# Kernel optimization log

Hardware: AMD Instinct MI355X
Metric: run time of the kernel (lower is better)

The kernel has to match this reference:

```python
import jax, jax.numpy as jnp
import numpy as np

N_DST = 100_000
N_SRC = 200_000
DEG = 16            # fixed avg degree -> E = N_DST*DEG
E = N_DST * DEG
P, K, W = 16, 256, 8  # num_parts, codebook entries, part width; feat_dim = P*W = 128
F_IN = P * W
F_OUT = 128


def setup_inputs() -> dict:
    key = jax.random.key(0)
    k1, k2, k3, k4, k5, k6, k7 = jax.random.split(key, 7)
    codes = jax.random.randint(k1, (N_SRC, P), 0, K, dtype=jnp.int32)
    indices = jax.random.randint(k2, (E,), 0, N_SRC, dtype=jnp.int32)
    indptr = (jnp.arange(N_DST + 1, dtype=jnp.int32) * DEG)
    h_self = jax.random.normal(k3, (N_DST, F_IN), dtype=jnp.float32)
    codebook = jax.random.normal(k4, (P, K, W), dtype=jnp.float32)
    W_neigh = jax.random.normal(k5, (F_OUT, F_IN), dtype=jnp.float32) * (1.0 / np.sqrt(F_IN))
    W_self = jax.random.normal(k6, (F_OUT, F_IN), dtype=jnp.float32) * (1.0 / np.sqrt(F_IN))
    b_self = jax.random.normal(k7, (F_OUT,), dtype=jnp.float32) * 0.01
    return {"codes": codes, "indices": indices, "indptr": indptr, "h_self": h_self,
            "codebook": codebook, "W_neigh": W_neigh, "W_self": W_self, "b_self": b_self}


def reference(codes, indices, indptr, h_self, codebook, W_neigh, W_self, b_self):
    n_dst = indptr.shape[0] - 1
    n_edges = indices.shape[0]
    # --- VQ decompress: codebook[p, codes[n, p]] -> [N_src, P, W] -> [N_src, F_IN]
    feat = codebook[jnp.arange(P)[None, :], codes]          # [N_src, P, W]
    feat = feat.reshape(feat.shape[0], F_IN)                # [N_src, F_IN]
    # --- CSR(CSC) mean SpMM over neighbors
    # dst id of each edge from indptr (jit-safe, static E)
    dst_ids = jnp.searchsorted(indptr, jnp.arange(n_edges, dtype=indptr.dtype), side="right") - 1
    gathered = feat[indices]                                 # [E, F_IN] (irregular gather)
    summed = jax.ops.segment_sum(gathered, dst_ids, num_segments=n_dst)  # [N_dst, F_IN]
    deg = jnp.diff(indptr).astype(summed.dtype)
    h_neigh = summed / jnp.maximum(deg, 1.0)[:, None]        # mean aggregation
    # --- linear combine: fc_neigh(h_neigh) + fc_self(h_self)
    rst = h_neigh @ W_neigh.T + h_self @ W_self.T + b_self[None, :]
    return rst
```

## Files before the change

kernel.cpp:

```cpp
#include <hip/hip_runtime.h>
#include <stdint.h>

constexpr int N_DST = 100000;
constexpr int N_SRC = 200000;
constexpr int DEG   = 16;
constexpr int PP    = 16;
constexpr int KK    = 256;
constexpr int WW    = 8;
constexpr int F_IN  = 128;
constexpr int F_OUT = 128;

typedef __attribute__((ext_vector_type(8))) short short8;
typedef __attribute__((ext_vector_type(4))) float floatx4;

__device__ __forceinline__ unsigned short f2bf(float f) {
    unsigned int u = __float_as_uint(f);
    unsigned int r = (u + 0x7FFFu + ((u >> 16) & 1u)) >> 16;
    return (unsigned short)r;
}
__device__ __forceinline__ float bf2f(unsigned int bits16) {
    return __uint_as_float(bits16 << 16);
}

constexpr int DT = 64;
constexpr int NT = (N_DST + DT - 1) / DT;
constexpr int LDS_STRIDE = 264;

__global__ __launch_bounds__(1024, 1) void fused_kernel(
    const int* __restrict__ codes, const int* __restrict__ indices,
    const float* __restrict__ codebook, const float* __restrict__ h_self,
    const float* __restrict__ Wn, const float* __restrict__ Ws,
    const float* __restrict__ b_self, float* __restrict__ out)
{
    __shared__ __align__(16) unsigned short scb[PP * KK * WW];
    __shared__ __align__(16) unsigned short hcat[DT][LDS_STRIDE];

    const int tid  = threadIdx.x;
    const int wv   = tid >> 6;
    const int lane = tid & 63;
    const int quad = lane >> 4;
    const int r    = lane & 15;
    const int p    = lane & 15;
    const int sub  = lane >> 4;

    {
        const float4* cb4 = (const float4*)codebook;
        ushort4* s4 = (ushort4*)scb;
        #pragma unroll
        for (int it = 0; it < 8; ++it) {
            const int i = tid + it * 1024;
            const float4 v = cb4[i];
            ushort4 w;
            w.x = f2bf(v.x); w.y = f2bf(v.y); w.z = f2bf(v.z); w.w = f2bf(v.w);
            s4[i] = w;
        }
    }

    const int cg = wv & 7;
    const int rg = wv >> 3;
    short8 bfrag[8];
    #pragma unroll
    for (int kt = 0; kt < 8; ++kt) {
        const int o  = cg * 16 + r;
        const int kb = kt * 32 + quad * 8;
        const float* src = (kb < 128) ? (Wn + o * 128 + kb)
                                      : (Ws + o * 128 + (kb - 128));
        union { short8 v; unsigned short u[8]; } f;
        #pragma unroll
        for (int j = 0; j < 8; ++j) f.u[j] = f2bf(src[j]);
        bfrag[kt] = f.v;
    }
    const float bs = b_self[cg * 16 + r];

    __syncthreads();

    for (int tile = blockIdx.x; tile < NT; tile += gridDim.x) {
        const int d0 = tile * DT;

        const int dbase = d0 + wv * 4;
        int sidx = 0;
        if (dbase + sub < N_DST) sidx = indices[dbase * DEG + lane];

        float4 hv[2];
        int hdl[2], hkq[2];
        #pragma unroll
        for (int it = 0; it < 2; ++it) {
            const int j  = tid + it * 1024;
            hdl[it] = j >> 5; hkq[it] = j & 31;
            const int d  = d0 + hdl[it];
            hv[it] = make_float4(0.f, 0.f, 0.f, 0.f);
            if (d < N_DST) hv[it] = ((const float4*)h_self)[(size_t)d * 32 + hkq[it]];
        }

        int c[16];
        #pragma unroll
        for (int e = 0; e < 16; ++e) {
            const int s = __shfl(sidx, (lane & 48) | e, 64);
            c[e] = codes[s * PP + p];
        }

        float ga[8];
        #pragma unroll
        for (int i = 0; i < 8; ++i) ga[i] = 0.f;
        #pragma unroll
        for (int e = 0; e < 16; ++e) {
            const uint4 q = *(const uint4*)(scb + (((p << 8) | c[e]) << 3));
            ga[0] += bf2f(q.x & 0xFFFFu);
            ga[1] += bf2f(q.x >> 16);
            ga[2] += bf2f(q.y & 0xFFFFu);
            ga[3] += bf2f(q.y >> 16);
            ga[4] += bf2f(q.z & 0xFFFFu);
            ga[5] += bf2f(q.z >> 16);
            ga[6] += bf2f(q.w & 0xFFFFu);
            ga[7] += bf2f(q.w >> 16);
        }

        {
            uint4 o4;
            o4.x = (unsigned int)f2bf(ga[0] * 0.0625f) | ((unsigned int)f2bf(ga[1] * 0.0625f) << 16);
            o4.y = (unsigned int)f2bf(ga[2] * 0.0625f) | ((unsigned int)f2bf(ga[3] * 0.0625f) << 16);
            o4.z = (unsigned int)f2bf(ga[4] * 0.0625f) | ((unsigned int)f2bf(ga[5] * 0.0625f) << 16);
            o4.w = (unsigned int)f2bf(ga[6] * 0.0625f) | ((unsigned int)f2bf(ga[7] * 0.0625f) << 16);
            *(uint4*)&hcat[wv * 4 + sub][p * 8] = o4;
        }
        #pragma unroll
        for (int it = 0; it < 2; ++it) {
            const unsigned int w0 = (unsigned int)f2bf(hv[it].x) | ((unsigned int)f2bf(hv[it].y) << 16);
            const unsigned int w1 = (unsigned int)f2bf(hv[it].z) | ((unsigned int)f2bf(hv[it].w) << 16);
            unsigned int* pr = (unsigned int*)&hcat[hdl[it]][128];
            pr[hkq[it] * 2]     = w0;
            pr[hkq[it] * 2 + 1] = w1;
        }
        __syncthreads();

        floatx4 acc[2];
        acc[0] = (floatx4)(0.f);
        acc[1] = (floatx4)(0.f);
        #pragma unroll
        for (int kt = 0; kt < 8; ++kt) {
            const short8 a0 = *(const short8*)&hcat[rg * 32 + r][kt * 32 + quad * 8];
            const short8 a1 = *(const short8*)&hcat[rg * 32 + 16 + r][kt * 32 + quad * 8];
            acc[0] = __builtin_amdgcn_mfma_f32_16x16x32_bf16(a0, bfrag[kt], acc[0], 0, 0, 0);
            acc[1] = __builtin_amdgcn_mfma_f32_16x16x32_bf16(a1, bfrag[kt], acc[1], 0, 0, 0);
        }

        #pragma unroll
        for (int m = 0; m < 2; ++m) {
            #pragma unroll
            for (int e = 0; e < 4; ++e) {
                const int d = d0 + rg * 32 + m * 16 + quad * 4 + e;
                if (d < N_DST) out[(size_t)d * F_OUT + cg * 16 + r] = acc[m][e] + bs;
            }
        }
        __syncthreads();
    }
}

extern "C" void kernel_launch(void* const* d_in, const int* in_sizes, int n_in,
                              void* d_out, int out_size, void* d_ws, size_t ws_size,
                              hipStream_t stream) {
    const int*   codes    = (const int*)d_in[0];
    const int*   indices  = (const int*)d_in[1];
    const float* h_self   = (const float*)d_in[3];
    const float* codebook = (const float*)d_in[4];
    const float* W_neigh  = (const float*)d_in[5];
    const float* W_self   = (const float*)d_in[6];
    const float* b_self   = (const float*)d_in[7];
    float*       out      = (float*)d_out;

    fused_kernel<<<256, 1024, 0, stream>>>(codes, indices, codebook, h_self,
                                           W_neigh, W_self, b_self, out);
}
```

Baseline: 163.5 us.

## Software-pipeline index/code gathers and double-buffer LDS tile to drop a barrier

Restructures the persistent tile loop so that the neighbor indices are prefetched two tiles ahead and the codes are gathered one tile ahead. This hides the dependent global-gather latency behind the current tile's LDS decode and MFMA work. The hcat staging buffer is double-buffered, which lets the trailing __syncthreads be removed. The h_self load is rewritten so each thread handles 8 contiguous floats. The changes add register pressure from two 16-element code arrays. The launch_bounds min-blocks hint rises from 1 to 4, which is unachievable with about 98KB of LDS per 1024-thread block and may tighten register limits or cause spills.

```diff
diff --git a/kernel.cpp b/kernel.cpp
--- a/kernel.cpp
+++ b/kernel.cpp
@@ -26,14 +26,14 @@
 constexpr int NT = (N_DST + DT - 1) / DT;
 constexpr int LDS_STRIDE = 264;
 
-__global__ __launch_bounds__(1024, 1) void fused_kernel(
+__global__ __launch_bounds__(1024, 4) void fused_kernel(
     const int* __restrict__ codes, const int* __restrict__ indices,
     const float* __restrict__ codebook, const float* __restrict__ h_self,
     const float* __restrict__ Wn, const float* __restrict__ Ws,
     const float* __restrict__ b_self, float* __restrict__ out)
 {
     __shared__ __align__(16) unsigned short scb[PP * KK * WW];
-    __shared__ __align__(16) unsigned short hcat[DT][LDS_STRIDE];
+    __shared__ __align__(16) unsigned short hcat[2][DT][LDS_STRIDE];
 
     const int tid  = threadIdx.x;
     const int wv   = tid >> 6;
@@ -74,37 +74,64 @@
 
     __syncthreads();
 
-    for (int tile = blockIdx.x; tile < NT; tile += gridDim.x) {
-        const int d0 = tile * DT;
-
-        const int dbase = d0 + wv * 4;
-        int sidx = 0;
-        if (dbase + sub < N_DST) sidx = indices[dbase * DEG + lane];
-
-        float4 hv[2];
-        int hdl[2], hkq[2];
-        #pragma unroll
-        for (int it = 0; it < 2; ++it) {
-            const int j  = tid + it * 1024;
-            hdl[it] = j >> 5; hkq[it] = j & 31;
-            const int d  = d0 + hdl[it];
-            hv[it] = make_float4(0.f, 0.f, 0.f, 0.f);
-            if (d < N_DST) hv[it] = ((const float4*)h_self)[(size_t)d * 32 + hkq[it]];
-        }
-
-        int c[16];
+    const int G = gridDim.x;
+    int t = blockIdx.x;
+
+    int sidx_cur = 0;
+    {
+        const int db = t * DT + wv * 4;
+        if (db + sub < N_DST) sidx_cur = indices[db * DEG + lane];
+    }
+    int sidx_nxt = 0;
+    if (t + G < NT) {
+        const int db = (t + G) * DT + wv * 4;
+        if (db + sub < N_DST) sidx_nxt = indices[db * DEG + lane];
+    }
+    int c_cur[16];
+    #pragma unroll
+    for (int e = 0; e < 16; ++e) {
+        const int s = __shfl(sidx_cur, (lane & 48) | e, 64);
+        c_cur[e] = codes[s * PP + p];
+    }
+
+    int buf = 0;
+    for (; t < NT; t += G) {
+        const int d0 = t * DT;
+
+        int sidx_nn = 0;
+        if (t + 2 * G < NT) {
+            const int db = (t + 2 * G) * DT + wv * 4;
+            if (db + sub < N_DST) sidx_nn = indices[db * DEG + lane];
+        }
+
+        int c_nxt[16];
+        if (t + G < NT) {
+            #pragma unroll
+            for (int e = 0; e < 16; ++e) {
+                const int s = __shfl(sidx_nxt, (lane & 48) | e, 64);
+                c_nxt[e] = codes[s * PP + p];
+            }
+        } else {
+            #pragma unroll
+            for (int e = 0; e < 16; ++e) c_nxt[e] = 0;
+        }
+
+        const int hrow = tid >> 4;
+        const int hcol = tid & 15;
+        const int hd   = d0 + hrow;
+        float4 ha = make_float4(0.f, 0.f, 0.f, 0.f);
+        float4 hb = ha;
+        if (hd < N_DST) {
+            const float4* s4 = (const float4*)(h_self + (size_t)hd * F_IN + hcol * 8);
+            ha = s4[0]; hb = s4[1];
+        }
+
+        float ga[8];
+        #pragma unroll
+        for (int i = 0; i < 8; ++i) ga[i] = 0.f;
         #pragma unroll
         for (int e = 0; e < 16; ++e) {
-            const int s = __shfl(sidx, (lane & 48) | e, 64);
-            c[e] = codes[s * PP + p];
-        }
-
-        float ga[8];
-        #pragma unroll
-        for (int i = 0; i < 8; ++i) ga[i] = 0.f;
-        #pragma unroll
-        for (int e = 0; e < 16; ++e) {
-            const uint4 q = *(const uint4*)(scb + (((p << 8) | c[e]) << 3));
+            const uint4 q = *(const uint4*)(scb + (((p << 8) | c_cur[e]) << 3));
             ga[0] += bf2f(q.x & 0xFFFFu);
             ga[1] += bf2f(q.x >> 16);
             ga[2] += bf2f(q.y & 0xFFFFu);
@@ -121,38 +148,45 @@
             o4.y = (unsigned int)f2bf(ga[2] * 0.0625f) | ((unsigned int)f2bf(ga[3] * 0.0625f) << 16);
             o4.z = (unsigned int)f2bf(ga[4] * 0.0625f) | ((unsigned int)f2bf(ga[5] * 0.0625f) << 16);
             o4.w = (unsigned int)f2bf(ga[6] * 0.0625f) | ((unsigned int)f2bf(ga[7] * 0.0625f) << 16);
-            *(uint4*)&hcat[wv * 4 + sub][p * 8] = o4;
-        }
-        #pragma unroll
-        for (int it = 0; it < 2; ++it) {
-            const unsigned int w0 = (unsigned int)f2bf(hv[it].x) | ((unsigned int)f2bf(hv[it].y) << 16);
-            const unsigned int w1 = (unsigned int)f2bf(hv[it].z) | ((unsigned int)f2bf(hv[it].w) << 16);
-            unsigned int* pr = (unsigned int*)&hcat[hdl[it]][128];
-            pr[hkq[it] * 2]     = w0;
-            pr[hkq[it] * 2 + 1] = w1;
-        }
+            *(uint4*)&hcat[buf][wv * 4 + sub][p * 8] = o4;
+        }
+
+        {
+            uint4 hw;
+            hw.x = (unsigned int)f2bf(ha.x) | ((unsigned int)f2bf(ha.y) << 16);
+            hw.y = (unsigned int)f2bf(ha.z) | ((unsigned int)f2bf(ha.w) << 16);
+            hw.z = (unsigned int)f2bf(hb.x) | ((unsigned int)f2bf(hb.y) << 16);
+            hw.w = (unsigned int)f2bf(hb.z) | ((unsigned int)f2bf(hb.w) << 16);
+            *(uint4*)&hcat[buf][hrow][128 + hcol * 8] = hw;
+        }
+
         __syncthreads();
 
-        floatx4 acc[2];
-        acc[0] = (floatx4)(0.f);
-        acc[1] = (floatx4)(0.f);
+        floatx4 acc0 = (floatx4)(0.f);
+        floatx4 acc1 = (floatx4)(0.f);
         #pragma unroll
         for (int kt = 0; kt < 8; ++kt) {
-            const short8 a0 = *(const short8*)&hcat[rg * 32 + r][kt * 32 + quad * 8];
-            const short8 a1 = *(const short8*)&hcat[rg * 32 + 16 + r][kt * 32 + quad * 8];
-            acc[0] = __builtin_amdgcn_mfma_f32_16x16x32_bf16(a0, bfrag[kt], acc[0], 0, 0, 0);
-            acc[1] = __builtin_amdgcn_mfma_f32_16x16x32_bf16(a1, bfrag[kt], acc[1], 0, 0, 0);
-        }
-
-        #pragma unroll
-        for (int m = 0; m < 2; ++m) {
-            #pragma unroll
-            for (int e = 0; e < 4; ++e) {
-                const int d = d0 + rg * 32 + m * 16 + quad * 4 + e;
-                if (d < N_DST) out[(size_t)d * F_OUT + cg * 16 + r] = acc[m][e] + bs;
-            }
-        }
-        __syncthreads();
+            const short8 a0 = *(const short8*)&hcat[buf][rg * 32 + r][kt * 32 + quad * 8];
+            const short8 a1 = *(const short8*)&hcat[buf][rg * 32 + 16 + r][kt * 32 + quad * 8];
+            acc0 = __builtin_amdgcn_mfma_f32_16x16x32_bf16(a0, bfrag[kt], acc0, 0, 0, 0);
+            acc1 = __builtin_amdgcn_mfma_f32_16x16x32_bf16(a1, bfrag[kt], acc1, 0, 0, 0);
+        }
+
+        #pragma unroll
+        for (int e = 0; e < 4; ++e) {
+            const int d = d0 + rg * 32 + quad * 4 + e;
+            if (d < N_DST) out[(size_t)d * F_OUT + cg * 16 + r] = acc0[e] + bs;
+        }
+        #pragma unroll
+        for (int e = 0; e < 4; ++e) {
+            const int d = d0 + rg * 32 + 16 + quad * 4 + e;
+            if (d < N_DST) out[(size_t)d * F_OUT + cg * 16 + r] = acc1[e] + bs;
+        }
+
+        #pragma unroll
+        for (int e = 0; e < 16; ++e) c_cur[e] = c_nxt[e];
+        sidx_nxt = sidx_nn;
+        buf ^= 1;
     }
 }
 
```

New measurement: 165.9 us. Within noise of the previous version (+1.5%).

## Make each wave own a 16-row stripe and pipeline code gathers without block barriers

Applied to the files above, without the earlier changes.

Work is now split per wave: each wave processes 16 destination rows end to end, so the per-tile __syncthreads are gone. Code loads for the next group of four rows are issued before the current group is accumulated, with sched_barriers to hold that order. The bf16 weights move into swizzled LDS and are read for all 8 column groups. h_self is fed to the MFMA straight from registers, and the codebook layout becomes k-major. The goal is to hide gather latency and remove block-wide syncs, at the cost of more LDS traffic for the weights, more register pressure, and a block size of 512 with 2 blocks per CU.

```diff
diff --git a/kernel.cpp b/kernel.cpp
--- a/kernel.cpp
+++ b/kernel.cpp
@@ -9,6 +9,7 @@
 constexpr int WW    = 8;
 constexpr int F_IN  = 128;
 constexpr int F_OUT = 128;
+constexpr int NSTRIPE = N_DST / 16;
 
 typedef __attribute__((ext_vector_type(8))) short short8;
 typedef __attribute__((ext_vector_type(4))) float floatx4;
@@ -18,22 +19,23 @@
     unsigned int r = (u + 0x7FFFu + ((u >> 16) & 1u)) >> 16;
     return (unsigned short)r;
 }
-__device__ __forceinline__ float bf2f(unsigned int bits16) {
-    return __uint_as_float(bits16 << 16);
+__device__ __forceinline__ float bf_lo(unsigned int q) {
+    return __uint_as_float(q << 16);
+}
+__device__ __forceinline__ float bf_hi(unsigned int q) {
+    return __uint_as_float(q & 0xFFFF0000u);
 }
 
-constexpr int DT = 64;
-constexpr int NT = (N_DST + DT - 1) / DT;
-constexpr int LDS_STRIDE = 264;
 
-__global__ __launch_bounds__(1024, 1) void fused_kernel(
+__global__ __launch_bounds__(512, 2) void fused_kernel(
     const int* __restrict__ codes, const int* __restrict__ indices,
     const float* __restrict__ codebook, const float* __restrict__ h_self,
     const float* __restrict__ Wn, const float* __restrict__ Ws,
     const float* __restrict__ b_self, float* __restrict__ out)
 {
-    __shared__ __align__(16) unsigned short scb[PP * KK * WW];
-    __shared__ __align__(16) unsigned short hcat[DT][LDS_STRIDE];
+    __shared__ __align__(16) unsigned short scb[KK * PP * WW];
+    __shared__ __align__(16) unsigned short wlds[F_OUT][256];
+    __shared__ __align__(16) unsigned short tbuf[8][16][128];
 
     const int tid  = threadIdx.x;
     const int wv   = tid >> 6;
@@ -47,112 +49,136 @@
         const float4* cb4 = (const float4*)codebook;
         ushort4* s4 = (ushort4*)scb;
         #pragma unroll
-        for (int it = 0; it < 8; ++it) {
-            const int i = tid + it * 1024;
+        for (int it = 0; it < 16; ++it) {
+            const int i = tid + it * 512;
             const float4 v = cb4[i];
+            const int pp_  = i >> 9;
+            const int k    = (i >> 1) & 255;
+            const int half = i & 1;
             ushort4 w;
             w.x = f2bf(v.x); w.y = f2bf(v.y); w.z = f2bf(v.z); w.w = f2bf(v.w);
-            s4[i] = w;
+            s4[((k << 4) | pp_) * 2 + half] = w;
         }
     }
 
-    const int cg = wv & 7;
-    const int rg = wv >> 3;
-    short8 bfrag[8];
     #pragma unroll
-    for (int kt = 0; kt < 8; ++kt) {
-        const int o  = cg * 16 + r;
-        const int kb = kt * 32 + quad * 8;
-        const float* src = (kb < 128) ? (Wn + o * 128 + kb)
-                                      : (Ws + o * 128 + (kb - 128));
-        union { short8 v; unsigned short u[8]; } f;
-        #pragma unroll
-        for (int j = 0; j < 8; ++j) f.u[j] = f2bf(src[j]);
-        bfrag[kt] = f.v;
+    for (int j = 0; j < 16; ++j) {
+        const int fi = tid + j * 512;
+        const int o  = fi >> 6;
+        const int fc = fi & 63;
+        const int k  = fc * 4;
+        const float* src = (k < 128) ? (Wn + o * 128 + k)
+                                     : (Ws + o * 128 + (k - 128));
+        const float4 v = *(const float4*)src;
+        ushort4 w;
+        w.x = f2bf(v.x); w.y = f2bf(v.y); w.z = f2bf(v.z); w.w = f2bf(v.w);
+        const int ch = fc >> 1;
+        const int hc = fc & 1;
+        *(ushort4*)&wlds[o][((ch ^ (o & 7)) << 3) + hc * 4] = w;
     }
-    const float bs = b_self[cg * 16 + r];
+
+    float bsv[8];
+    #pragma unroll
+    for (int cg = 0; cg < 8; ++cg) bsv[cg] = b_self[cg * 16 + r];
 
     __syncthreads();
 
-    for (int tile = blockIdx.x; tile < NT; tile += gridDim.x) {
-        const int d0 = tile * DT;
-
-        const int dbase = d0 + wv * 4;
-        int sidx = 0;
-        if (dbase + sub < N_DST) sidx = indices[dbase * DEG + lane];
-
-        float4 hv[2];
-        int hdl[2], hkq[2];
-        #pragma unroll
-        for (int it = 0; it < 2; ++it) {
-            const int j  = tid + it * 1024;
-            hdl[it] = j >> 5; hkq[it] = j & 31;
-            const int d  = d0 + hdl[it];
-            hv[it] = make_float4(0.f, 0.f, 0.f, 0.f);
-            if (d < N_DST) hv[it] = ((const float4*)h_self)[(size_t)d * 32 + hkq[it]];
-        }
-
-        int c[16];
+    auto issue_codes = [&](int sidx, int* cc) {
         #pragma unroll
         for (int e = 0; e < 16; ++e) {
             const int s = __shfl(sidx, (lane & 48) | e, 64);
-            c[e] = codes[s * PP + p];
+            cc[e] = codes[s * PP + p];
         }
-
+    };
+    auto do_unit = [&](const int* cc, int u) {
         float ga[8];
         #pragma unroll
         for (int i = 0; i < 8; ++i) ga[i] = 0.f;
         #pragma unroll
         for (int e = 0; e < 16; ++e) {
-            const uint4 q = *(const uint4*)(scb + (((p << 8) | c[e]) << 3));
-            ga[0] += bf2f(q.x & 0xFFFFu);
-            ga[1] += bf2f(q.x >> 16);
-            ga[2] += bf2f(q.y & 0xFFFFu);
-            ga[3] += bf2f(q.y >> 16);
-            ga[4] += bf2f(q.z & 0xFFFFu);
-            ga[5] += bf2f(q.z >> 16);
-            ga[6] += bf2f(q.w & 0xFFFFu);
-            ga[7] += bf2f(q.w >> 16);
+            const uint4 q = *(const uint4*)(scb + (((cc[e] << 4) | p) << 3));
+            ga[0] += bf_lo(q.x); ga[1] += bf_hi(q.x);
+            ga[2] += bf_lo(q.y); ga[3] += bf_hi(q.y);
+            ga[4] += bf_lo(q.z); ga[5] += bf_hi(q.z);
+            ga[6] += bf_lo(q.w); ga[7] += bf_hi(q.w);
+        }
+        const int ridx = u * 4 + sub;
+        uint4 o4;
+        o4.x = (unsigned int)f2bf(ga[0] * 0.0625f) | ((unsigned int)f2bf(ga[1] * 0.0625f) << 16);
+        o4.y = (unsigned int)f2bf(ga[2] * 0.0625f) | ((unsigned int)f2bf(ga[3] * 0.0625f) << 16);
+        o4.z = (unsigned int)f2bf(ga[4] * 0.0625f) | ((unsigned int)f2bf(ga[5] * 0.0625f) << 16);
+        o4.w = (unsigned int)f2bf(ga[6] * 0.0625f) | ((unsigned int)f2bf(ga[7] * 0.0625f) << 16);
+        *(uint4*)&tbuf[wv][ridx][(p ^ (ridx & 7)) << 3] = o4;
+    };
+
+    for (int s = blockIdx.x * 8 + wv; s < NSTRIPE; s += gridDim.x * 8) {
+        const int S0 = s * 16;
+
+        const int sidx0 = indices[(S0     ) * DEG + lane];
+        const int sidx1 = indices[(S0 +  4) * DEG + lane];
+        const int sidx2 = indices[(S0 +  8) * DEG + lane];
+        const int sidx3 = indices[(S0 + 12) * DEG + lane];
+        float4 hsv[8];
+        #pragma unroll
+        for (int k2 = 0; k2 < 4; ++k2) {
+            const float* hp = h_self + (size_t)(S0 + r) * F_IN + k2 * 32 + quad * 8;
+            hsv[k2 * 2]     = *(const float4*)hp;
+            hsv[k2 * 2 + 1] = *(const float4*)(hp + 4);
+        }
+        __builtin_amdgcn_sched_barrier(0);
+
+        int c0[16], c1[16], c2[16], c3[16];
+        issue_codes(sidx0, c0);
+        issue_codes(sidx1, c1);
+        __builtin_amdgcn_sched_barrier(0);
+        do_unit(c0, 0);
+        issue_codes(sidx2, c2);
+        __builtin_amdgcn_sched_barrier(0);
+        do_unit(c1, 1);
+        issue_codes(sidx3, c3);
+        __builtin_amdgcn_sched_barrier(0);
+        do_unit(c2, 2);
+        do_unit(c3, 3);
+
+        short8 af4[4];
+        #pragma unroll
+        for (int k2 = 0; k2 < 4; ++k2) {
+            union { short8 v; unsigned short u[8]; } f;
+            f.u[0] = f2bf(hsv[k2 * 2].x);     f.u[1] = f2bf(hsv[k2 * 2].y);
+            f.u[2] = f2bf(hsv[k2 * 2].z);     f.u[3] = f2bf(hsv[k2 * 2].w);
+            f.u[4] = f2bf(hsv[k2 * 2 + 1].x); f.u[5] = f2bf(hsv[k2 * 2 + 1].y);
+            f.u[6] = f2bf(hsv[k2 * 2 + 1].z); f.u[7] = f2bf(hsv[k2 * 2 + 1].w);
+            af4[k2] = f.v;
         }
 
-        {
-            uint4 o4;
-            o4.x = (unsigned int)f2bf(ga[0] * 0.0625f) | ((unsigned int)f2bf(ga[1] * 0.0625f) << 16);
-            o4.y = (unsigned int)f2bf(ga[2] * 0.0625f) | ((unsigned int)f2bf(ga[3] * 0.0625f) << 16);
-            o4.z = (unsigned int)f2bf(ga[4] * 0.0625f) | ((unsigned int)f2bf(ga[5] * 0.0625f) << 16);
-            o4.w = (unsigned int)f2bf(ga[6] * 0.0625f) | ((unsigned int)f2bf(ga[7] * 0.0625f) << 16);
-            *(uint4*)&hcat[wv * 4 + sub][p * 8] = o4;
-        }
+        floatx4 acc[8];
         #pragma unroll
-        for (int it = 0; it < 2; ++it) {
-            const unsigned int w0 = (unsigned int)f2bf(hv[it].x) | ((unsigned int)f2bf(hv[it].y) << 16);
-            const unsigned int w1 = (unsigned int)f2bf(hv[it].z) | ((unsigned int)f2bf(hv[it].w) << 16);
-            unsigned int* pr = (unsigned int*)&hcat[hdl[it]][128];
-            pr[hkq[it] * 2]     = w0;
-            pr[hkq[it] * 2 + 1] = w1;
-        }
-        __syncthreads();
-
-        floatx4 acc[2];
-        acc[0] = (floatx4)(0.f);
-        acc[1] = (floatx4)(0.f);
+        for (int cg = 0; cg < 8; ++cg) acc[cg] = (floatx4)(0.f);
         #pragma unroll
         for (int kt = 0; kt < 8; ++kt) {
-            const short8 a0 = *(const short8*)&hcat[rg * 32 + r][kt * 32 + quad * 8];
-            const short8 a1 = *(const short8*)&hcat[rg * 32 + 16 + r][kt * 32 + quad * 8];
-            acc[0] = __builtin_amdgcn_mfma_f32_16x16x32_bf16(a0, bfrag[kt], acc[0], 0, 0, 0);
-            acc[1] = __builtin_amdgcn_mfma_f32_16x16x32_bf16(a1, bfrag[kt], acc[1], 0, 0, 0);
+            short8 a;
+            if (kt < 4) {
+                a = *(const short8*)&tbuf[wv][r][((4 * kt + quad) ^ (r & 7)) << 3];
+            } else {
+                a = af4[kt - 4];
+            }
+            #pragma unroll
+            for (int cg = 0; cg < 8; ++cg) {
+                const int o = cg * 16 + r;
+                const short8 b = *(const short8*)
+                    &wlds[o][(((kt * 4 + quad) ^ (o & 7)) << 3)];
+                acc[cg] = __builtin_amdgcn_mfma_f32_16x16x32_bf16(a, b, acc[cg], 0, 0, 0);
+            }
         }
 
         #pragma unroll
-        for (int m = 0; m < 2; ++m) {
+        for (int cg = 0; cg < 8; ++cg) {
             #pragma unroll
             for (int e = 0; e < 4; ++e) {
-                const int d = d0 + rg * 32 + m * 16 + quad * 4 + e;
-                if (d < N_DST) out[(size_t)d * F_OUT + cg * 16 + r] = acc[m][e] + bs;
+                const int d = S0 + quad * 4 + e;
+                out[(size_t)d * F_OUT + cg * 16 + r] = acc[cg][e] + bsv[cg];
             }
         }
-        __syncthreads();
     }
 }
 
@@ -168,6 +194,6 @@
     const float* b_self   = (const float*)d_in[7];
     float*       out      = (float*)d_out;
 
-    fused_kernel<<<256, 1024, 0, stream>>>(codes, indices, codebook, h_self,
-                                           W_neigh, W_self, b_self, out);
+    fused_kernel<<<256, 512, 0, stream>>>(codes, indices, codebook, h_self,
+                                          W_neigh, W_self, b_self, out);
 }
```

Measured after the change: 155.6 us. -4.8%, faster.
